# Kernel optimization log

Hardware: AMD Instinct MI355X
Metric: run time of the kernel (lower is better)

Reference implementation:

```python
import jax, jax.numpy as jnp
import numpy as np

D = 64  # max disparity search range (d in the torch module)


def setup_inputs() -> dict:
    key = jax.random.key(0)
    k1, k2 = jax.random.split(key)
    B, C, H, W = 8, 128, 128, 256
    x1 = jax.random.normal(k1, (B, C, H, W), dtype=jnp.float32)
    x2 = jax.random.normal(k2, (B, C, H, W), dtype=jnp.float32)
    return {"x1": x1, "x2": x2}


def _corr_volume(x1, x2, d):
    # result[n, i, h, w] = (1/C) * sum_c x1[n,c,h,w] * x2[n,c,h,w-i], zero where w-i < 0
    n, c, h, w = x2.shape
    slices = []
    for i in range(d + 1):
        # shift x2 right by i columns, zero-padding on the left
        shifted = jnp.pad(x2[:, :, :, : w - i] if i > 0 else x2,
                          ((0, 0), (0, 0), (0, 0), (i, 0)))
        slices.append(jnp.sum(x1 * shifted, axis=1))  # [n, h, w]
    cv = jnp.stack(slices, axis=1)  # [n, d+1, h, w]
    return cv * (1.0 / c)


def reference(x1, x2):
    return _corr_volume(x1, x2, D)
```

## Files before the change

### kernel.cpp

```cpp
#include <hip/hip_runtime.h>
#include <hip/hip_fp16.h>


constexpr int B   = 8;
constexpr int C   = 128;
constexpr int H   = 128;
constexpr int W   = 256;
constexpr int NI  = 65;
constexpr int HW  = H * W;
constexpr int CHW = C * HW;
constexpr int KC2 = 8;
constexpr int X2W = 320;
constexpr int NCHUNK = C / (2 * KC2);

typedef _Float16 half2v __attribute__((ext_vector_type(2)));

__device__ inline unsigned int pack2(float a, float b) {
    __half2 h = __floats2half2_rn(a, b);
    return __builtin_bit_cast(unsigned int, h);
}

__device__ inline float fdot2f(unsigned int a, unsigned int b, float c) {
#if __has_builtin(__builtin_amdgcn_fdot2)
    return __builtin_amdgcn_fdot2(__builtin_bit_cast(half2v, a),
                                  __builtin_bit_cast(half2v, b), c, false);
#else
    __half2 ha = __builtin_bit_cast(__half2, a);
    __half2 hb = __builtin_bit_cast(__half2, b);
    float2 fa = __half22float2(ha), fb = __half22float2(hb);
    return fmaf(fa.x, fb.x, fmaf(fa.y, fb.y, c));
#endif
}

__global__ __launch_bounds__(256, 3)
void corr_volume_kernel(const float* __restrict__ x1,
                        const float* __restrict__ x2,
                        float* __restrict__ out) {
    const int h   = blockIdx.x;
    const int n   = blockIdx.y;
    const int tid = threadIdx.x;
    const int l   = tid & 63;
    const int qi  = tid >> 6;

    __shared__ unsigned int x2h[2][KC2][X2W];

    float acc[16][4];
    #pragma unroll
    for (int il = 0; il < 16; ++il)
        #pragma unroll
        for (int wl = 0; wl < 4; ++wl) acc[il][wl] = 0.0f;
    float acc64[4] = {0.f, 0.f, 0.f, 0.f};

    const int j0a = 4 * l - 16 * qi + 48;

    const float* x1g = x1 + n * CHW + h * W;
    const float* x2g = x2 + n * CHW + h * W;

    {
        const int bufi = tid >> 7;
        const int r    = (tid >> 4) & 7;
        const int cq   = tid & 15;
        *(uint4*)&x2h[bufi][r][4 * cq] = make_uint4(0u, 0u, 0u, 0u);
    }

    float4 L[4];
    auto issue = [&](int c0) {
        #pragma unroll
        for (int rr = 0; rr < 2; ++rr) {
            const int r = 2 * qi + rr;
            const float* g = x2g + (c0 + 2 * r) * HW + 4 * l;
            L[2 * rr + 0] = *(const float4*)g;
            L[2 * rr + 1] = *(const float4*)(g + HW);
        }
    };
    auto commit = [&](int bufi) {
        #pragma unroll
        for (int rr = 0; rr < 2; ++rr) {
            const int r = 2 * qi + rr;
            uint4 p;
            p.x = pack2(L[2 * rr].x, L[2 * rr + 1].x);
            p.y = pack2(L[2 * rr].y, L[2 * rr + 1].y);
            p.z = pack2(L[2 * rr].z, L[2 * rr + 1].z);
            p.w = pack2(L[2 * rr].w, L[2 * rr + 1].w);
            *(uint4*)&x2h[bufi][r][64 + 4 * l] = p;
        }
    };

    issue(0);
    commit(0);
    __syncthreads();

    for (int t = 0; t < NCHUNK; ++t) {
        const int cur = t & 1;
        const int c0  = t * 2 * KC2;

        if (t + 1 < NCHUNK) issue((t + 1) * 2 * KC2);
        asm volatile("" ::: "memory");

        #pragma unroll 2
        for (int c2 = 0; c2 < KC2; ++c2) {
            const float4 lo = *(const float4*)(x1g + (c0 + 2 * c2) * HW + 4 * l);
            const float4 hi = *(const float4*)(x1g + (c0 + 2 * c2 + 1) * HW + 4 * l);
            const unsigned int aw[4] = {pack2(lo.x, hi.x), pack2(lo.y, hi.y),
                                        pack2(lo.z, hi.z), pack2(lo.w, hi.w)};
            const uint4 b0 = *(const uint4*)&x2h[cur][c2][j0a];
            const uint4 b1 = *(const uint4*)&x2h[cur][c2][j0a + 4];
            const uint4 b2 = *(const uint4*)&x2h[cur][c2][j0a + 8];
            const uint4 b3 = *(const uint4*)&x2h[cur][c2][j0a + 12];
            const uint4 b4 = *(const uint4*)&x2h[cur][c2][j0a + 16];
            const unsigned int bw[20] = {b0.x, b0.y, b0.z, b0.w,
                                         b1.x, b1.y, b1.z, b1.w,
                                         b2.x, b2.y, b2.z, b2.w,
                                         b3.x, b3.y, b3.z, b3.w,
                                         b4.x, b4.y, b4.z, b4.w};
            #pragma unroll
            for (int il = 0; il < 16; ++il)
                #pragma unroll
                for (int wl = 0; wl < 4; ++wl)
                    acc[il][wl] = fdot2f(aw[wl], bw[16 + wl - il], acc[il][wl]);

            if (qi == 3) {
                #pragma unroll
                for (int wl = 0; wl < 4; ++wl)
                    acc64[wl] = fdot2f(aw[wl], bw[wl], acc64[wl]);
            }
        }

        if (t + 1 < NCHUNK) {
            commit((t + 1) & 1);
            __syncthreads();
        }
    }

    const float scale = 1.0f / (float)C;
    float* outg = out + n * (NI * HW) + h * W + 4 * l;
    #pragma unroll
    for (int il = 0; il < 16; ++il) {
        const int i = 16 * qi + il;
        *(float4*)(outg + i * HW) =
            make_float4(acc[il][0] * scale, acc[il][1] * scale,
                        acc[il][2] * scale, acc[il][3] * scale);
    }
    if (qi == 3) {
        *(float4*)(outg + 64 * HW) =
            make_float4(acc64[0] * scale, acc64[1] * scale,
                        acc64[2] * scale, acc64[3] * scale);
    }
}

extern "C" void kernel_launch(void* const* d_in, const int* in_sizes, int n_in,
                              void* d_out, int out_size, void* d_ws, size_t ws_size,
                              hipStream_t stream) {
    const float* x1 = (const float*)d_in[0];
    const float* x2 = (const float*)d_in[1];
    float* out = (float*)d_out;
    dim3 grid(H, B);
    corr_volume_kernel<<<grid, 256, 0, stream>>>(x1, x2, out);
}
```

Baseline: 333.0 us.

## Split each row block into single-wave blocks and software-pipeline x1/x2 loads

Each 256-thread block is replaced by four 64-thread single-wave blocks, one per disparity quarter. Each wave stages the whole fp16-packed x2 row into its own LDS double buffer, so the block-wide __syncthreads disappears. The x1 loads are also moved into a register prefetch pipeline that overlaps with the dot-product work, and the channel chunk is halved. The cost is four times the x2 global and L2 traffic plus four times as many blocks, and the code now depends on in-order LDS access within a single wave.

```diff
diff --git a/kernel.cpp b/kernel.cpp
--- a/kernel.cpp
+++ b/kernel.cpp
@@ -9,8 +9,8 @@
 constexpr int NI  = 65;
 constexpr int HW  = H * W;
 constexpr int CHW = C * HW;
-constexpr int KC2 = 8;
-constexpr int X2W = 320;
+constexpr int KC2 = 4;
+constexpr int X2W = 324;
 constexpr int NCHUNK = C / (2 * KC2);
 
 typedef _Float16 half2v __attribute__((ext_vector_type(2)));
@@ -32,15 +32,14 @@
 #endif
 }
 
-__global__ __launch_bounds__(256, 3)
+__global__ __launch_bounds__(64, 3)
 void corr_volume_kernel(const float* __restrict__ x1,
                         const float* __restrict__ x2,
                         float* __restrict__ out) {
-    const int h   = blockIdx.x;
-    const int n   = blockIdx.y;
-    const int tid = threadIdx.x;
-    const int l   = tid & 63;
-    const int qi  = tid >> 6;
+    const int qi = blockIdx.x;
+    const int h  = blockIdx.y;
+    const int n  = blockIdx.z;
+    const int l  = threadIdx.x;
 
     __shared__ unsigned int x2h[2][KC2][X2W];
 
@@ -56,80 +55,113 @@
     const float* x1g = x1 + n * CHW + h * W;
     const float* x2g = x2 + n * CHW + h * W;
 
-    {
-        const int bufi = tid >> 7;
-        const int r    = (tid >> 4) & 7;
-        const int cq   = tid & 15;
+    #pragma unroll
+    for (int k = 0; k < 2; ++k) {
+        const int idx  = l + 64 * k;
+        const int bufi = idx >> 6;
+        const int r    = (idx >> 4) & 3;
+        const int cq   = idx & 15;
         *(uint4*)&x2h[bufi][r][4 * cq] = make_uint4(0u, 0u, 0u, 0u);
     }
 
-    float4 L[4];
-    auto issue = [&](int c0) {
+    const int sr = l >> 4;
+    const int ss = l & 15;
+
+    float4 R2[8];
+    auto issueX2 = [&](int c0) {
         #pragma unroll
-        for (int rr = 0; rr < 2; ++rr) {
-            const int r = 2 * qi + rr;
-            const float* g = x2g + (c0 + 2 * r) * HW + 4 * l;
-            L[2 * rr + 0] = *(const float4*)g;
-            L[2 * rr + 1] = *(const float4*)(g + HW);
+        for (int k = 0; k < 4; ++k) {
+            const float* g = x2g + (c0 + 2 * sr) * HW + 4 * (ss + 16 * k);
+            R2[2 * k]     = *(const float4*)g;
+            R2[2 * k + 1] = *(const float4*)(g + HW);
         }
     };
-    auto commit = [&](int bufi) {
+    auto commitX2 = [&](int bufi) {
         #pragma unroll
-        for (int rr = 0; rr < 2; ++rr) {
-            const int r = 2 * qi + rr;
+        for (int k = 0; k < 4; ++k) {
             uint4 p;
-            p.x = pack2(L[2 * rr].x, L[2 * rr + 1].x);
-            p.y = pack2(L[2 * rr].y, L[2 * rr + 1].y);
-            p.z = pack2(L[2 * rr].z, L[2 * rr + 1].z);
-            p.w = pack2(L[2 * rr].w, L[2 * rr + 1].w);
-            *(uint4*)&x2h[bufi][r][64 + 4 * l] = p;
+            p.x = pack2(R2[2 * k].x, R2[2 * k + 1].x);
+            p.y = pack2(R2[2 * k].y, R2[2 * k + 1].y);
+            p.z = pack2(R2[2 * k].z, R2[2 * k + 1].z);
+            p.w = pack2(R2[2 * k].w, R2[2 * k + 1].w);
+            *(uint4*)&x2h[bufi][sr][64 + 4 * (ss + 16 * k)] = p;
         }
     };
 
-    issue(0);
-    commit(0);
-    __syncthreads();
+    float4 R1[4];
+    unsigned int aw[4][4];
+    auto issueX1 = [&](int c0, int p0) {
+        #pragma unroll
+        for (int pp = 0; pp < 2; ++pp) {
+            const float* g = x1g + (c0 + 2 * (p0 + pp)) * HW + 4 * l;
+            R1[2 * pp]     = *(const float4*)g;
+            R1[2 * pp + 1] = *(const float4*)(g + HW);
+        }
+    };
+    auto packX1 = [&](int p0) {
+        #pragma unroll
+        for (int pp = 0; pp < 2; ++pp) {
+            const float4 lo = R1[2 * pp], hi = R1[2 * pp + 1];
+            aw[p0 + pp][0] = pack2(lo.x, hi.x);
+            aw[p0 + pp][1] = pack2(lo.y, hi.y);
+            aw[p0 + pp][2] = pack2(lo.z, hi.z);
+            aw[p0 + pp][3] = pack2(lo.w, hi.w);
+        }
+    };
+
+    auto computeC2 = [&](int bufi, int c2) {
+        const uint4 b0 = *(const uint4*)&x2h[bufi][c2][j0a];
+        const uint4 b1 = *(const uint4*)&x2h[bufi][c2][j0a + 4];
+        const uint4 b2 = *(const uint4*)&x2h[bufi][c2][j0a + 8];
+        const uint4 b3 = *(const uint4*)&x2h[bufi][c2][j0a + 12];
+        const uint4 b4 = *(const uint4*)&x2h[bufi][c2][j0a + 16];
+        const unsigned int bw[20] = {b0.x, b0.y, b0.z, b0.w,
+                                     b1.x, b1.y, b1.z, b1.w,
+                                     b2.x, b2.y, b2.z, b2.w,
+                                     b3.x, b3.y, b3.z, b3.w,
+                                     b4.x, b4.y, b4.z, b4.w};
+        #pragma unroll
+        for (int il = 0; il < 16; ++il)
+            #pragma unroll
+            for (int wl = 0; wl < 4; ++wl)
+                acc[il][wl] = fdot2f(aw[c2][wl], bw[16 + wl - il], acc[il][wl]);
+        if (qi == 3) {
+            #pragma unroll
+            for (int wl = 0; wl < 4; ++wl)
+                acc64[wl] = fdot2f(aw[c2][wl], bw[wl], acc64[wl]);
+        }
+    };
+
+    issueX2(0);
+    issueX1(0, 0);
+    commitX2(0);
+    packX1(0);
+    issueX1(0, 2);
+    packX1(2);
+    asm volatile("" ::: "memory");
 
     for (int t = 0; t < NCHUNK; ++t) {
-        const int cur = t & 1;
-        const int c0  = t * 2 * KC2;
+        const int cur  = t & 1;
+        const int c0n  = (t + 1) * 2 * KC2;
+        const bool more = (t + 1 < NCHUNK);
 
-        if (t + 1 < NCHUNK) issue((t + 1) * 2 * KC2);
+        if (more) { issueX2(c0n); issueX1(c0n, 0); }
         asm volatile("" ::: "memory");
 
-        #pragma unroll 2
-        for (int c2 = 0; c2 < KC2; ++c2) {
-            const float4 lo = *(const float4*)(x1g + (c0 + 2 * c2) * HW + 4 * l);
-            const float4 hi = *(const float4*)(x1g + (c0 + 2 * c2 + 1) * HW + 4 * l);
-            const unsigned int aw[4] = {pack2(lo.x, hi.x), pack2(lo.y, hi.y),
-                                        pack2(lo.z, hi.z), pack2(lo.w, hi.w)};
-            const uint4 b0 = *(const uint4*)&x2h[cur][c2][j0a];
-            const uint4 b1 = *(const uint4*)&x2h[cur][c2][j0a + 4];
-            const uint4 b2 = *(const uint4*)&x2h[cur][c2][j0a + 8];
-            const uint4 b3 = *(const uint4*)&x2h[cur][c2][j0a + 12];
-            const uint4 b4 = *(const uint4*)&x2h[cur][c2][j0a + 16];
-            const unsigned int bw[20] = {b0.x, b0.y, b0.z, b0.w,
-                                         b1.x, b1.y, b1.z, b1.w,
-                                         b2.x, b2.y, b2.z, b2.w,
-                                         b3.x, b3.y, b3.z, b3.w,
-                                         b4.x, b4.y, b4.z, b4.w};
-            #pragma unroll
-            for (int il = 0; il < 16; ++il)
-                #pragma unroll
-                for (int wl = 0; wl < 4; ++wl)
-                    acc[il][wl] = fdot2f(aw[wl], bw[16 + wl - il], acc[il][wl]);
+        computeC2(cur, 0);
+        computeC2(cur, 1);
 
-            if (qi == 3) {
-                #pragma unroll
-                for (int wl = 0; wl < 4; ++wl)
-                    acc64[wl] = fdot2f(aw[wl], bw[wl], acc64[wl]);
-            }
+        if (more) { packX1(0); issueX1(c0n, 2); }
+        asm volatile("" ::: "memory");
+
+        computeC2(cur, 2);
+        computeC2(cur, 3);
+
+        if (more) {
+            commitX2(cur ^ 1);
+            packX1(2);
         }
-
-        if (t + 1 < NCHUNK) {
-            commit((t + 1) & 1);
-            __syncthreads();
-        }
+        asm volatile("" ::: "memory");
     }
 
     const float scale = 1.0f / (float)C;
@@ -154,6 +186,6 @@
     const float* x1 = (const float*)d_in[0];
     const float* x2 = (const float*)d_in[1];
     float* out = (float*)d_out;
-    dim3 grid(H, B);
-    corr_volume_kernel<<<grid, 256, 0, stream>>>(x1, x2, out);
+    dim3 grid(4, H, B);
+    corr_volume_kernel<<<grid, 64, 0, stream>>>(x1, x2, out);
 }
```

Result: slower. 838.1 us (+151.7%).
